# Performance work log

Hardware: AMD Instinct MI355X
Metric: run time of the kernel (lower is better)

Reference implementation:

```python
import jax, jax.numpy as jnp
import numpy as np

L = 2        # num_layers
D = 512      # d_model
H = 8        # heads
C = 512      # GAT per-head out channels (= d_model, concat=False -> mean over heads)
B, S, E = 4, 512, 4096
NEG = jnp.float32(-1e9)


def setup_inputs() -> dict:
    key = jax.random.key(0)
    ks = jax.random.split(key, 20)
    sc = 0.02  # weight init scale
    inp = {
        'x': jax.random.normal(ks[0], (B, S, D), jnp.float32),
        'Wq': jax.random.normal(ks[1], (L, D, D), jnp.float32) * sc,
        'bq': jnp.zeros((L, D), jnp.float32),
        'Wk': jax.random.normal(ks[2], (L, D, D), jnp.float32) * sc,
        'bk': jnp.zeros((L, D), jnp.float32),
        'Wv': jax.random.normal(ks[3], (L, D, D), jnp.float32) * sc,
        'bv': jnp.zeros((L, D), jnp.float32),
        'Wo': jax.random.normal(ks[4], (L, D, D), jnp.float32) * sc,
        'bo': jnp.zeros((L, D), jnp.float32),
        'gatW': jax.random.normal(ks[5], (L, D, H * C), jnp.float32) * sc,
        'att_src': jax.random.normal(ks[6], (L, H, C), jnp.float32) * sc,
        'att_dst': jax.random.normal(ks[7], (L, H, C), jnp.float32) * sc,
        'gat_bias': jnp.zeros((L, C), jnp.float32),
        'ln_g': jnp.ones((L, D), jnp.float32),
        'ln_b': jnp.zeros((L, D), jnp.float32),
        'input_len': jax.random.randint(ks[8], (B,), S // 2, S + 1, jnp.int32),
        'edges': jax.random.randint(ks[9], (B, 2, E), 0, S // 2, jnp.int32),
        'edge_num': jax.random.randint(ks[10], (B,), E // 2, E + 1, jnp.int32),
    }
    return inp


def layer_norm(x, g, b, eps=1e-5):
    m = x.mean(-1, keepdims=True)
    v = ((x - m) ** 2).mean(-1, keepdims=True)
    return (x - m) * jax.lax.rsqrt(v + eps) * g + b


def mha(x, pad_mask, Wq, bq, Wk, bk, Wv, bv, Wo, bo):
    # pad_mask: [B,S] True where padded (masked out)
    b, s, d = x.shape
    dh = d // H
    q = (x @ Wq + bq).reshape(b, s, H, dh)
    k = (x @ Wk + bk).reshape(b, s, H, dh)
    v = (x @ Wv + bv).reshape(b, s, H, dh)
    scores = jnp.einsum('bqhd,bkhd->bhqk', q, k) / jnp.float32(np.sqrt(dh))
    scores = jnp.where(pad_mask[:, None, None, :], NEG, scores)
    a = jax.nn.softmax(scores, axis=-1)
    o = jnp.einsum('bhqk,bkhd->bqhd', a, v).reshape(b, s, d)
    return o @ Wo + bo


def gat_single(x, edge_index, edge_mask, node_mask, W, a_src_w, a_dst_w, bias):
    # x: [S,D]; edge_index: [2,E]; GATConv(d_model,d_model,heads,concat=False)
    s = x.shape[0]
    h = (x @ W).reshape(s, H, C)
    a_src_n = (h * a_src_w).sum(-1)  # [S,H]
    a_dst_n = (h * a_dst_w).sum(-1)  # [S,H]
    # add self loops (PyG default) for valid nodes
    ar = jnp.arange(s, dtype=edge_index.dtype)
    src = jnp.concatenate([edge_index[0], ar])
    dst = jnp.concatenate([edge_index[1], ar])
    em = jnp.concatenate([edge_mask, node_mask])  # [E+S]
    alpha = jax.nn.leaky_relu(a_src_n[src] + a_dst_n[dst], 0.2)  # [E+S,H]
    alpha = jnp.where(em[:, None], alpha, NEG)
    amax = jax.ops.segment_max(alpha, dst, num_segments=s)  # [S,H]
    ex = jnp.exp(alpha - amax[dst]) * em[:, None].astype(alpha.dtype)
    denom = jax.ops.segment_sum(ex, dst, num_segments=s)
    coef = ex / (denom[dst] + 1e-16)
    msg = h[src] * coef[:, :, None]  # [E+S,H,C]
    out = jax.ops.segment_sum(msg, dst, num_segments=s)  # [S,H,C]
    return out.mean(axis=1) + bias  # concat=False -> mean over heads


def reference(x, Wq, bq, Wk, bk, Wv, bv, Wo, bo, gatW, att_src, att_dst,
              gat_bias, ln_g, ln_b, input_len, edges, edge_num):
    b, s, d = x.shape
    node_mask = jnp.arange(s)[None, :] < input_len[:, None]      # [B,S]
    edge_mask = jnp.arange(edges.shape[-1])[None, :] < edge_num[:, None]  # [B,E]
    pad_mask = ~node_mask
    out = x
    layer_outputs = []
    gat_b = jax.vmap(gat_single, in_axes=(0, 0, 0, 0, None, None, None, None))
    for i in range(L):
        out = mha(out, pad_mask, Wq[i], bq[i], Wk[i], bk[i], Wv[i], bv[i], Wo[i], bo[i])
        g = gat_b(out, edges, edge_mask, node_mask,
                  gatW[i], att_src[i], att_dst[i], gat_bias[i])
        y = jax.nn.relu(layer_norm(g, ln_g[i], ln_b[i])) + out
        out = jnp.where(node_mask[:, :, None], y, out)
        layer_outputs.append(out)
    return jnp.stack(layer_outputs)  # [L,B,S,D]
```

## Files before the change

kernel.cpp:

```cpp
#include <hip/hip_runtime.h>
#include <cstddef>

#define DMODEL 512
#define HEADS  8
#define DH     64
#define CCH    512
#define BATCH  4
#define SEQ    512
#define NEDGE  4096
#define NLAYER 2
#define HC     (HEADS*CCH)

typedef unsigned short bf16_t;
typedef __attribute__((ext_vector_type(8))) short short8;
typedef __attribute__((ext_vector_type(4))) float floatx4;

__device__ __forceinline__ bf16_t f2bf(float f){
  unsigned u = __float_as_uint(f);
  unsigned r = (u + 0x7FFFu + ((u>>16)&1u)) >> 16;
  return (bf16_t)r;
}
__device__ __forceinline__ float bf2f(bf16_t u){ return __uint_as_float(((unsigned)u)<<16); }

__global__ void k_f2b(const float* __restrict__ in, bf16_t* __restrict__ out, int n4){
  int i = blockIdx.x*256 + threadIdx.x;
  if (i < n4){
    float4 v = ((const float4*)in)[i];
    ushort4 o;
    o.x=f2bf(v.x); o.y=f2bf(v.y); o.z=f2bf(v.z); o.w=f2bf(v.w);
    ((ushort4*)out)[i]=o;
  }
}

__global__ __launch_bounds__(256) void k_edges(const int* __restrict__ edges,
    const int* __restrict__ edge_num, int* __restrict__ cnt, int* __restrict__ offs,
    int* __restrict__ elist, float* __restrict__ attn_nodes, int an_total){
  __shared__ int cnt_l[SEQ];
  __shared__ int off_l[SEQ];
  __shared__ int cur_l[SEQ];
  int b = blockIdx.x, tid = threadIdx.x;
  int chunk = an_total / BATCH;
  for (int i = tid; i < chunk; i += 256) attn_nodes[b*chunk + i] = 0.f;
  for (int s = tid; s < SEQ; s += 256) cnt_l[s] = 0;
  __syncthreads();
  int ne = edge_num[b];
  const int* dstrow = edges + (size_t)b*2*NEDGE + NEDGE;
  for (int e = tid; e < ne; e += 256) atomicAdd(&cnt_l[dstrow[e]], 1);
  __syncthreads();
  if (tid == 0){
    int acc = 0;
    for (int s = 0; s < SEQ; s++){ off_l[s] = acc; acc += cnt_l[s]; }
  }
  __syncthreads();
  for (int s = tid; s < SEQ; s += 256) cur_l[s] = off_l[s];
  __syncthreads();
  for (int e = tid; e < ne; e += 256){
    int dst = dstrow[e];
    int pos = atomicAdd(&cur_l[dst], 1);
    elist[(size_t)b*NEDGE + pos] = e;
  }
  for (int s = tid; s < SEQ; s += 256){
    cnt[b*SEQ + s]  = cnt_l[s];
    offs[b*SEQ + s] = off_l[s];
  }
}

struct WtJob { const float* W[10]; bf16_t* WT[10]; };
__global__ __launch_bounds__(256) void k_wt_all(WtJob j){
  __shared__ float T[32][65];
  int t = blockIdx.x, k0 = blockIdx.y*32;
  int wsel, n0, N;
  if (t < 64){ wsel = t>>3; n0 = (t&7)*64; N = 512; }
  else { int t2 = t-64; wsel = 8 + (t2>>6); n0 = (t2&63)*64; N = 4096; }
  const float* W = j.W[wsel];
  bf16_t* WT = j.WT[wsel];
  const int K = 512;
  int tid = threadIdx.x;
  int lk = tid>>3, ln = (tid&7)*8;
  const float* src = W + (size_t)(k0+lk)*N + n0 + ln;
  float4 v0 = *(const float4*)src;
  float4 v1 = *(const float4*)(src+4);
  T[lk][ln+0]=v0.x; T[lk][ln+1]=v0.y; T[lk][ln+2]=v0.z; T[lk][ln+3]=v0.w;
  T[lk][ln+4]=v1.x; T[lk][ln+5]=v1.y; T[lk][ln+6]=v1.z; T[lk][ln+7]=v1.w;
  __syncthreads();
  int wn = tid>>2, wk = (tid&3)*8;
  ushort4 o0, o1;
  o0.x=f2bf(T[wk+0][wn]); o0.y=f2bf(T[wk+1][wn]); o0.z=f2bf(T[wk+2][wn]); o0.w=f2bf(T[wk+3][wn]);
  o1.x=f2bf(T[wk+4][wn]); o1.y=f2bf(T[wk+5][wn]); o1.z=f2bf(T[wk+6][wn]); o1.w=f2bf(T[wk+7][wn]);
  bf16_t* dst = WT + (size_t)(n0+wn)*K + k0 + wk;
  *(ushort4*)dst = o0;
  *(ushort4*)(dst+4) = o1;
}

struct GemmB {
  const bf16_t* W; const float* bias; float* C; bf16_t* Cb;
  const float* att_s; const float* att_d; float* asrc; float* adst;
};
struct GemmB3 { GemmB g[3]; };

__global__ __launch_bounds__(256) void k_gemm_mfma(const bf16_t* __restrict__ A, GemmB3 p,
                                                   int N, int K){
  const GemmB& g = p.g[blockIdx.z];
  const bf16_t* Wt  = g.W;
  const float* bias = g.bias;
  float* C          = g.C;
  bf16_t* Cb        = g.Cb;
  __shared__ __align__(16) bf16_t As[2][64*64];
  __shared__ __align__(16) bf16_t Bs[2][64*64];
  int bm = blockIdx.x*64, bn = blockIdx.y*64;
  int tid = threadIdx.x;
  int wave = tid>>6, lane = tid&63;
  int wy = wave>>1, wx = wave&1;
  int quad = lane>>4, l16 = lane&15;
  int l7 = l16&7;
  floatx4 acc[2][2];
  #pragma unroll
  for (int i=0;i<2;i++)
    #pragma unroll
    for (int j=0;j<2;j++) acc[i][j] = (floatx4){0.f,0.f,0.f,0.f};
  int sr = tid>>2;
  int sch = (tid&3)*2;
  int sc = sch<<3;
  int wof0 = sr*64 + ((sch     ^ (sr&7))<<3);
  int wof1 = sr*64 + (((sch+1) ^ (sr&7))<<3);
  const bf16_t* Aptr = A  + (size_t)(bm+sr)*K + sc;
  const bf16_t* Bptr = Wt + (size_t)(bn+sr)*K + sc;
  uint4 a0, a1, b0, b1;
  a0 = *(const uint4*)(Aptr);     a1 = *(const uint4*)(Aptr + 8);
  b0 = *(const uint4*)(Bptr);     b1 = *(const uint4*)(Bptr + 8);
  *(uint4*)(As[0] + wof0) = a0;
  *(uint4*)(As[0] + wof1) = a1;
  *(uint4*)(Bs[0] + wof0) = b0;
  *(uint4*)(Bs[0] + wof1) = b1;
  int rch0 = (quad ^ l7)<<3;
  int rch1 = rch0 ^ 32;
  const int nk = K>>6;
  for (int k=0; k<nk; k++){
    __syncthreads();
    if (k+1 < nk){
      int ko = (k+1)<<6;
      a0 = *(const uint4*)(Aptr + ko);     a1 = *(const uint4*)(Aptr + ko + 8);
      b0 = *(const uint4*)(Bptr + ko);     b1 = *(const uint4*)(Bptr + ko + 8);
    }
    const bf16_t* Ab = As[k&1];
    const bf16_t* Bb = Bs[k&1];
    short8 af[2][2], bfr[2][2];
    #pragma unroll
    for (int i=0;i<2;i++){
      int ra = (wy*32+i*16+l16)*64;
      af[0][i] = *(const short8*)(Ab + ra + rch0);
      af[1][i] = *(const short8*)(Ab + ra + rch1);
    }
    #pragma unroll
    for (int j=0;j<2;j++){
      int rb = (wx*32+j*16+l16)*64;
      bfr[0][j] = *(const short8*)(Bb + rb + rch0);
      bfr[1][j] = *(const short8*)(Bb + rb + rch1);
    }
    #pragma unroll
    for (int i=0;i<2;i++)
      #pragma unroll
      for (int j=0;j<2;j++){
        acc[i][j] = __builtin_amdgcn_mfma_f32_16x16x32_bf16(af[0][i], bfr[0][j], acc[i][j], 0,0,0);
        acc[i][j] = __builtin_amdgcn_mfma_f32_16x16x32_bf16(af[1][i], bfr[1][j], acc[i][j], 0,0,0);
      }
    if (k+1 < nk){
      bf16_t* Aw = As[(k+1)&1];
      bf16_t* Bw = Bs[(k+1)&1];
      *(uint4*)(Aw + wof0) = a0;
      *(uint4*)(Aw + wof1) = a1;
      *(uint4*)(Bw + wof0) = b0;
      *(uint4*)(Bw + wof1) = b1;
    }
  }
  #pragma unroll
  for (int i=0;i<2;i++){
    int row = bm + wy*32 + i*16 + quad*4;
    #pragma unroll
    for (int j=0;j<2;j++){
      int col = bn + wx*32 + j*16 + l16;
      float bi = bias ? bias[col] : 0.f;
      #pragma unroll
      for (int r=0;r<4;r++){
        float vvv = acc[i][j][r] + bi;
        if (C)  C[(size_t)(row+r)*N + col] = vvv;
        if (Cb) Cb[(size_t)(row+r)*N + col] = f2bf(vvv);
      }
    }
  }
  if (g.asrc){
    int colbase = bn + wx*32;
    int hidx = colbase >> 9;
    float aw_s[2], aw_d[2];
    #pragma unroll
    for (int j=0;j<2;j++){
      int col = colbase + j*16 + l16;
      aw_s[j] = g.att_s[col];
      aw_d[j] = g.att_d[col];
    }
    #pragma unroll
    for (int i=0;i<2;i++){
      #pragma unroll
      for (int r=0;r<4;r++){
        float ps=0.f, pd=0.f;
        #pragma unroll
        for (int j=0;j<2;j++){ ps += acc[i][j][r]*aw_s[j]; pd += acc[i][j][r]*aw_d[j]; }
        #pragma unroll
        for (int m2=1;m2<16;m2<<=1){ ps += __shfl_xor(ps,m2); pd += __shfl_xor(pd,m2); }
        if (l16==0){
          int row = bm + wy*32 + i*16 + quad*4 + r;
          atomicAdd(&g.asrc[row*HEADS + hidx], ps);
          atomicAdd(&g.adst[row*HEADS + hidx], pd);
        }
      }
    }
  }
}

__global__ __launch_bounds__(256) void k_attn_flash(const bf16_t* __restrict__ q,
    const bf16_t* __restrict__ k, const bf16_t* __restrict__ v,
    const int* __restrict__ input_len, bf16_t* __restrict__ o){
  __shared__ __align__(16) bf16_t Kt[64*72];
  __shared__ __align__(16) bf16_t Vt[64*72];
  __shared__ __align__(16) bf16_t Pt[4][16*72];
  int q0 = blockIdx.x*64;
  int h  = blockIdx.y, b = blockIdx.z;
  int len = input_len[b];
  int tid = threadIdx.x;
  int w = tid>>6, lane = tid&63;
  int quad = lane>>4, l16 = lane&15;
  const bf16_t* qrow = q + ((size_t)(b*SEQ + q0 + w*16 + l16))*DMODEL + h*DH;
  short8 qa0 = *(const short8*)(qrow + quad*8);
  short8 qa1 = *(const short8*)(qrow + quad*8 + 32);
  int kr = tid>>2, kc = (tid&3)<<4;
  int vr = lane,   vc = w<<4;
  const bf16_t* kbase = k + ((size_t)(b*SEQ))*DMODEL + h*DH;
  const bf16_t* vbase = v + ((size_t)(b*SEQ))*DMODEL + h*DH;
  floatx4 oacc[4];
  #pragma unroll
  for (int dt=0;dt<4;dt++) oacc[dt] = (floatx4){0.f,0.f,0.f,0.f};
  float mrun[4], lrun[4];
  #pragma unroll
  for (int r=0;r<4;r++){ mrun[r]=-1e30f; lrun[r]=0.f; }
  for (int kt=0; kt<SEQ; kt+=64){
    if (kt >= len) break;
    uint4 kv0 = *(const uint4*)(kbase + (size_t)(kt+kr)*DMODEL + kc);
    uint4 kv1 = *(const uint4*)(kbase + (size_t)(kt+kr)*DMODEL + kc + 8);
    uint4 vv0 = *(const uint4*)(vbase + (size_t)(kt+vr)*DMODEL + vc);
    uint4 vv1 = *(const uint4*)(vbase + (size_t)(kt+vr)*DMODEL + vc + 8);
    __syncthreads();
    *(uint4*)(Kt + kr*72 + kc)     = kv0;
    *(uint4*)(Kt + kr*72 + kc + 8) = kv1;
    const ushort* vp0 = (const ushort*)&vv0;
    const ushort* vp1 = (const ushort*)&vv1;
    #pragma unroll
    for (int i2=0;i2<8;i2++) Vt[(vc+i2)*72 + vr]   = vp0[i2];
    #pragma unroll
    for (int i2=0;i2<8;i2++) Vt[(vc+8+i2)*72 + vr] = vp1[i2];
    __syncthreads();
    floatx4 sacc[4];
    #pragma unroll
    for (int nt=0;nt<4;nt++){
      sacc[nt] = (floatx4){0.f,0.f,0.f,0.f};
      short8 kb0 = *(const short8*)(Kt + (nt*16+l16)*72 + quad*8);
      short8 kb1 = *(const short8*)(Kt + (nt*16+l16)*72 + quad*8 + 32);
      sacc[nt] = __builtin_amdgcn_mfma_f32_16x16x32_bf16(qa0, kb0, sacc[nt], 0,0,0);
      sacc[nt] = __builtin_amdgcn_mfma_f32_16x16x32_bf16(qa1, kb1, sacc[nt], 0,0,0);
    }
    #pragma unroll
    for (int nt=0;nt<4;nt++){
      bool valid = (kt + nt*16 + l16) < len;
      #pragma unroll
      for (int r=0;r<4;r++){
        float sv = sacc[nt][r]*0.125f;
        sacc[nt][r] = valid ? sv : -1e30f;
      }
    }
    float alpha[4];
    #pragma unroll
    for (int r=0;r<4;r++){
      float mx = fmaxf(fmaxf(sacc[0][r],sacc[1][r]), fmaxf(sacc[2][r],sacc[3][r]));
      #pragma unroll
      for (int off=1; off<16; off<<=1) mx = fmaxf(mx, __shfl_xor(mx, off));
      float mn = fmaxf(mrun[r], mx);
      alpha[r] = __expf(mrun[r]-mn);
      mrun[r] = mn;
      float rs = 0.f;
      #pragma unroll
      for (int nt=0;nt<4;nt++){
        float pp = __expf(sacc[nt][r]-mn);
        sacc[nt][r] = pp; rs += pp;
      }
      #pragma unroll
      for (int off=1; off<16; off<<=1) rs += __shfl_xor(rs, off);
      lrun[r] = lrun[r]*alpha[r] + rs;
    }
    #pragma unroll
    for (int dt=0;dt<4;dt++)
      #pragma unroll
      for (int r=0;r<4;r++) oacc[dt][r] *= alpha[r];
    bf16_t* pw = Pt[w];
    #pragma unroll
    for (int nt=0;nt<4;nt++)
      #pragma unroll
      for (int r=0;r<4;r++) pw[(quad*4+r)*72 + nt*16 + l16] = f2bf(sacc[nt][r]);
    short8 pa0 = *(const short8*)(pw + l16*72 + quad*8);
    short8 pa1 = *(const short8*)(pw + l16*72 + quad*8 + 32);
    #pragma unroll
    for (int dt=0;dt<4;dt++){
      short8 vb0 = *(const short8*)(Vt + (dt*16+l16)*72 + quad*8);
      short8 vb1 = *(const short8*)(Vt + (dt*16+l16)*72 + quad*8 + 32);
      oacc[dt] = __builtin_amdgcn_mfma_f32_16x16x32_bf16(pa0, vb0, oacc[dt], 0,0,0);
      oacc[dt] = __builtin_amdgcn_mfma_f32_16x16x32_bf16(pa1, vb1, oacc[dt], 0,0,0);
    }
  }
  bf16_t* obase = o + ((size_t)(b*SEQ + q0 + w*16 + quad*4))*DMODEL + h*DH;
  #pragma unroll
  for (int r=0;r<4;r++){
    float invl = 1.f/lrun[r];
    #pragma unroll
    for (int dt=0;dt<4;dt++)
      obase[(size_t)r*DMODEL + dt*16 + l16] = f2bf(oacc[dt][r]*invl);
  }
}

__global__ __launch_bounds__(256) void k_gat_ln(const bf16_t* __restrict__ hbuf,
    const float* __restrict__ asrc, const float* __restrict__ adst,
    const int* __restrict__ offs, const int* __restrict__ cnt, const int* __restrict__ elist,
    const int* __restrict__ edges, const int* __restrict__ input_len,
    const float* __restrict__ gat_bias, const float* __restrict__ mha,
    const float* __restrict__ lng, const float* __restrict__ lnb,
    bf16_t* __restrict__ curb, float* __restrict__ outp){
  int s = blockIdx.x, b = blockIdx.y;
  int tid = threadIdx.x;
  size_t row = ((size_t)(b*SEQ+s))*DMODEL;
  int c0 = tid*2;
  float2 xv = *(const float2*)(mha + row + c0);
  if (s >= input_len[b]){
    curb[row+c0]   = f2bf(xv.x);
    curb[row+c0+1] = f2bf(xv.y);
    *(float2*)(outp + row + c0) = xv;
    return;
  }
  __shared__ float amax_s[8], den_s[8], adl[8];
  __shared__ float cf[32][8];
  __shared__ int   cs[32];
  __shared__ float red[256];
  int n = cnt[b*SEQ+s];
  const int* el = elist + (size_t)b*NEDGE + offs[b*SEQ+s];
  const int* srcrow = edges + (size_t)b*2*NEDGE;
  if (tid < 8) adl[tid] = adst[(b*SEQ+s)*HEADS + tid];
  __syncthreads();
  if (tid < 64){
    float mx[8];
    #pragma unroll
    for (int h2=0;h2<8;h2++) mx[h2] = -1e30f;
    for (int j = tid; j <= n; j += 64){
      int src = (j==n) ? s : srcrow[el[j]];
      const float* ap = asrc + (size_t)(b*SEQ+src)*HEADS;
      #pragma unroll
      for (int h2=0;h2<8;h2++){
        float a = ap[h2] + adl[h2];
        a = (a>0.f)? a : 0.2f*a;
        mx[h2] = fmaxf(mx[h2], a);
      }
    }
    #pragma unroll
    for (int h2=0;h2<8;h2++){
      float vmx = mx[h2];
      #pragma unroll
      for (int off=32; off; off>>=1) vmx = fmaxf(vmx, __shfl_xor(vmx,off,64));
      mx[h2]=vmx;
    }
    float sm[8];
    #pragma unroll
    for (int h2=0;h2<8;h2++) sm[h2]=0.f;
    for (int j = tid; j <= n; j += 64){
      int src = (j==n) ? s : srcrow[el[j]];
      const float* ap = asrc + (size_t)(b*SEQ+src)*HEADS;
      #pragma unroll
      for (int h2=0;h2<8;h2++){
        float a = ap[h2] + adl[h2];
        a = (a>0.f)? a : 0.2f*a;
        sm[h2] += __expf(a - mx[h2]);
      }
    }
    #pragma unroll
    for (int h2=0;h2<8;h2++){
      float vs = sm[h2];
      #pragma unroll
      for (int off=32; off; off>>=1) vs += __shfl_xor(vs,off,64);
      if (tid==0){ amax_s[h2]=mx[h2]; den_s[h2]=vs; }
    }
  }
  __syncthreads();
  float acc0=0.f, acc1=0.f;
  for (int j0=0; j0 <= n; j0 += 32){
    int jm = min(32, n+1-j0);
    if (tid < jm*8){
      int jj = j0 + (tid>>3), h2 = tid&7;
      int src = (jj==n) ? s : srcrow[el[jj]];
      if (h2==0) cs[tid>>3] = src;
      float a = asrc[(size_t)(b*SEQ+src)*HEADS + h2] + adl[h2];
      a = (a>0.f)? a : 0.2f*a;
      cf[tid>>3][h2] = __expf(a - amax_s[h2]) / (den_s[h2] + 1e-16f);
    }
    __syncthreads();
    for (int jj=0; jj<jm; ++jj){
      int src = cs[jj];
      const bf16_t* hrow = hbuf + ((size_t)(b*SEQ+src))*HC;
      #pragma unroll
      for (int h2=0;h2<8;h2++){
        float wgt = cf[jj][h2];
        ushort2 hv = *(const ushort2*)(hrow + h2*CCH + c0);
        acc0 += wgt * bf2f(hv.x);
        acc1 += wgt * bf2f(hv.y);
      }
    }
    __syncthreads();
  }
  float g0 = acc0*0.125f + gat_bias[c0];
  float g1 = acc1*0.125f + gat_bias[c0+1];
  red[tid] = g0+g1;
  __syncthreads();
  for (int off=128; off; off>>=1){ if (tid<off) red[tid]+=red[tid+off]; __syncthreads(); }
  float mean = red[0]*(1.f/512.f);
  __syncthreads();
  float d0 = g0-mean, d1 = g1-mean;
  red[tid] = d0*d0 + d1*d1;
  __syncthreads();
  for (int off=128; off; off>>=1){ if (tid<off) red[tid]+=red[tid+off]; __syncthreads(); }
  float inv = rsqrtf(red[0]*(1.f/512.f) + 1e-5f);
  float t0 = d0*inv*lng[c0]   + lnb[c0];
  float t1 = d1*inv*lng[c0+1] + lnb[c0+1];
  float y0 = fmaxf(t0,0.f) + xv.x;
  float y1 = fmaxf(t1,0.f) + xv.y;
  curb[row+c0]   = f2bf(y0);
  curb[row+c0+1] = f2bf(y1);
  float2 outv = { y0, y1 };
  *(float2*)(outp + row + c0) = outv;
}

extern "C" void kernel_launch(void* const* d_in, const int* in_sizes, int n_in,
                              void* d_out, int out_size, void* d_ws, size_t ws_size,
                              hipStream_t stream){
  (void)in_sizes; (void)n_in; (void)out_size; (void)ws_size;
  const float* x       = (const float*)d_in[0];
  const float* Wq      = (const float*)d_in[1];
  const float* bq      = (const float*)d_in[2];
  const float* Wk      = (const float*)d_in[3];
  const float* bk      = (const float*)d_in[4];
  const float* Wv      = (const float*)d_in[5];
  const float* bv      = (const float*)d_in[6];
  const float* Wo      = (const float*)d_in[7];
  const float* bo      = (const float*)d_in[8];
  const float* gatW    = (const float*)d_in[9];
  const float* att_src = (const float*)d_in[10];
  const float* att_dst = (const float*)d_in[11];
  const float* gat_bias= (const float*)d_in[12];
  const float* ln_g    = (const float*)d_in[13];
  const float* ln_b    = (const float*)d_in[14];
  const int* input_len  = (const int*)d_in[15];
  const int* edges      = (const int*)d_in[16];
  const int* edge_num   = (const int*)d_in[17];
  float* outp = (float*)d_out;

  char* w = (char*)d_ws;
  size_t off = 0;
  auto alloc = [&](size_t bytes)->char*{ char* p = w + off; off += (bytes + 255) & ~(size_t)255; return p; };
  const size_t BSD = (size_t)BATCH*SEQ*DMODEL;
  const size_t BSH = (size_t)BATCH*SEQ*HEADS;
  float* mha  = (float*)alloc(BSD*4);
  bf16_t* hb  = (bf16_t*)alloc((size_t)BATCH*SEQ*HC*2);
  float* attn_nodes = (float*)alloc((size_t)NLAYER*2*BSH*4);
  int* cnt    = (int*)alloc(BATCH*SEQ*4);
  int* offs   = (int*)alloc(BATCH*SEQ*4);
  int* elist  = (int*)alloc((size_t)BATCH*NEDGE*4);
  bf16_t* xbf  = (bf16_t*)alloc(BSD*2);
  bf16_t* curb = (bf16_t*)alloc(BSD*2);
  bf16_t* qbf  = (bf16_t*)alloc(BSD*2);
  bf16_t* kbf  = (bf16_t*)alloc(BSD*2);
  bf16_t* vbf  = (bf16_t*)alloc(BSD*2);
  bf16_t* obf  = (bf16_t*)alloc(BSD*2);
  bf16_t* abf  = (bf16_t*)alloc(BSD*2);
  bf16_t* wqt  = (bf16_t*)alloc((size_t)NLAYER*DMODEL*DMODEL*2);
  bf16_t* wkt  = (bf16_t*)alloc((size_t)NLAYER*DMODEL*DMODEL*2);
  bf16_t* wvt  = (bf16_t*)alloc((size_t)NLAYER*DMODEL*DMODEL*2);
  bf16_t* wot  = (bf16_t*)alloc((size_t)NLAYER*DMODEL*DMODEL*2);
  bf16_t* gwt  = (bf16_t*)alloc((size_t)NLAYER*DMODEL*HC*2);

  k_edges<<<dim3(BATCH),256,0,stream>>>(edges, edge_num, cnt, offs, elist,
                                        attn_nodes, (int)(NLAYER*2*BSH));
  WtJob wj;
  for (int i=0;i<NLAYER;i++){
    size_t wo = (size_t)i*DMODEL*DMODEL;
    wj.W[i*4+0]=Wq+wo;  wj.WT[i*4+0]=wqt+wo;
    wj.W[i*4+1]=Wk+wo;  wj.WT[i*4+1]=wkt+wo;
    wj.W[i*4+2]=Wv+wo;  wj.WT[i*4+2]=wvt+wo;
    wj.W[i*4+3]=Wo+wo;  wj.WT[i*4+3]=wot+wo;
    size_t go = (size_t)i*DMODEL*HC;
    wj.W[8+i]=gatW+go;  wj.WT[8+i]=gwt+go;
  }
  k_wt_all<<<dim3(192, 16),256,0,stream>>>(wj);
  k_f2b<<<dim3((unsigned)(BSD/4/256)),256,0,stream>>>(x, xbf, (int)(BSD/4));

  const int M = BATCH*SEQ;
  for (int i=0;i<NLAYER;i++){
    size_t wo = (size_t)i*DMODEL*DMODEL;
    size_t bo2 = (size_t)i*DMODEL;
    float* asrc = attn_nodes + (size_t)i*2*BSH;
    float* adst = asrc + BSH;
    const bf16_t* Ab = (i==0) ? xbf : curb;
    GemmB3 qkv;
    qkv.g[0] = { wqt+wo, bq+bo2, nullptr, qbf, nullptr, nullptr, nullptr, nullptr };
    qkv.g[1] = { wkt+wo, bk+bo2, nullptr, kbf, nullptr, nullptr, nullptr, nullptr };
    qkv.g[2] = { wvt+wo, bv+bo2, nullptr, vbf, nullptr, nullptr, nullptr, nullptr };
    k_gemm_mfma<<<dim3(M/64, DMODEL/64, 3),256,0,stream>>>(Ab, qkv, DMODEL, DMODEL);
    k_attn_flash<<<dim3(SEQ/64, HEADS, BATCH),256,0,stream>>>(qbf, kbf, vbf, input_len, obf);
    GemmB3 og;
    og.g[0] = { wot+wo, bo+bo2, mha, abf, nullptr, nullptr, nullptr, nullptr };
    og.g[1] = og.g[0]; og.g[2] = og.g[0];
    k_gemm_mfma<<<dim3(M/64, DMODEL/64, 1),256,0,stream>>>(obf, og, DMODEL, DMODEL);
    GemmB3 gg;
    gg.g[0] = { gwt + (size_t)i*DMODEL*HC, nullptr, nullptr, hb,
                att_src + (size_t)i*HC, att_dst + (size_t)i*HC, asrc, adst };
    gg.g[1] = gg.g[0]; gg.g[2] = gg.g[0];
    k_gemm_mfma<<<dim3(M/64, HC/64, 1),256,0,stream>>>(abf, gg, HC, DMODEL);
    k_gat_ln<<<dim3(SEQ, BATCH),256,0,stream>>>(hb, asrc, adst, offs, cnt, elist, edges,
        input_len, gat_bias + (size_t)i*CCH, mha, ln_g+bo2, ln_b+bo2,
        curb, outp + (size_t)i*BSD);
  }
}
```

Baseline: 313.8 us.

## Split attention keys across warp pairs and merge preprocessing kernels into one launch

```diff
diff --git a/kernel.cpp b/kernel.cpp
--- a/kernel.cpp
+++ b/kernel.cpp
@@ -22,74 +22,75 @@
 }
 __device__ __forceinline__ float bf2f(bf16_t u){ return __uint_as_float(((unsigned)u)<<16); }
 
-__global__ void k_f2b(const float* __restrict__ in, bf16_t* __restrict__ out, int n4){
-  int i = blockIdx.x*256 + threadIdx.x;
-  if (i < n4){
-    float4 v = ((const float4*)in)[i];
-    ushort4 o;
-    o.x=f2bf(v.x); o.y=f2bf(v.y); o.z=f2bf(v.z); o.w=f2bf(v.w);
-    ((ushort4*)out)[i]=o;
-  }
-}
-
-__global__ __launch_bounds__(256) void k_edges(const int* __restrict__ edges,
+struct WtJob { const float* W[10]; bf16_t* WT[10]; };
+__global__ __launch_bounds__(256) void k_pre(const int* __restrict__ edges,
     const int* __restrict__ edge_num, int* __restrict__ cnt, int* __restrict__ offs,
-    int* __restrict__ elist, float* __restrict__ attn_nodes, int an_total){
+    int* __restrict__ elist, float* __restrict__ attn_nodes, int an_total,
+    WtJob j, const float* __restrict__ x, bf16_t* __restrict__ xbf, int n4){
   __shared__ int cnt_l[SEQ];
   __shared__ int off_l[SEQ];
   __shared__ int cur_l[SEQ];
-  int b = blockIdx.x, tid = threadIdx.x;
-  int chunk = an_total / BATCH;
-  for (int i = tid; i < chunk; i += 256) attn_nodes[b*chunk + i] = 0.f;
-  for (int s = tid; s < SEQ; s += 256) cnt_l[s] = 0;
-  __syncthreads();
-  int ne = edge_num[b];
-  const int* dstrow = edges + (size_t)b*2*NEDGE + NEDGE;
-  for (int e = tid; e < ne; e += 256) atomicAdd(&cnt_l[dstrow[e]], 1);
-  __syncthreads();
-  if (tid == 0){
-    int acc = 0;
-    for (int s = 0; s < SEQ; s++){ off_l[s] = acc; acc += cnt_l[s]; }
-  }
-  __syncthreads();
-  for (int s = tid; s < SEQ; s += 256) cur_l[s] = off_l[s];
-  __syncthreads();
-  for (int e = tid; e < ne; e += 256){
-    int dst = dstrow[e];
-    int pos = atomicAdd(&cur_l[dst], 1);
-    elist[(size_t)b*NEDGE + pos] = e;
-  }
-  for (int s = tid; s < SEQ; s += 256){
-    cnt[b*SEQ + s]  = cnt_l[s];
-    offs[b*SEQ + s] = off_l[s];
-  }
-}
-
-struct WtJob { const float* W[10]; bf16_t* WT[10]; };
-__global__ __launch_bounds__(256) void k_wt_all(WtJob j){
   __shared__ float T[32][65];
-  int t = blockIdx.x, k0 = blockIdx.y*32;
-  int wsel, n0, N;
-  if (t < 64){ wsel = t>>3; n0 = (t&7)*64; N = 512; }
-  else { int t2 = t-64; wsel = 8 + (t2>>6); n0 = (t2&63)*64; N = 4096; }
-  const float* W = j.W[wsel];
-  bf16_t* WT = j.WT[wsel];
-  const int K = 512;
-  int tid = threadIdx.x;
-  int lk = tid>>3, ln = (tid&7)*8;
-  const float* src = W + (size_t)(k0+lk)*N + n0 + ln;
-  float4 v0 = *(const float4*)src;
-  float4 v1 = *(const float4*)(src+4);
-  T[lk][ln+0]=v0.x; T[lk][ln+1]=v0.y; T[lk][ln+2]=v0.z; T[lk][ln+3]=v0.w;
-  T[lk][ln+4]=v1.x; T[lk][ln+5]=v1.y; T[lk][ln+6]=v1.z; T[lk][ln+7]=v1.w;
-  __syncthreads();
-  int wn = tid>>2, wk = (tid&3)*8;
-  ushort4 o0, o1;
-  o0.x=f2bf(T[wk+0][wn]); o0.y=f2bf(T[wk+1][wn]); o0.z=f2bf(T[wk+2][wn]); o0.w=f2bf(T[wk+3][wn]);
-  o1.x=f2bf(T[wk+4][wn]); o1.y=f2bf(T[wk+5][wn]); o1.z=f2bf(T[wk+6][wn]); o1.w=f2bf(T[wk+7][wn]);
-  bf16_t* dst = WT + (size_t)(n0+wn)*K + k0 + wk;
-  *(ushort4*)dst = o0;
-  *(ushort4*)(dst+4) = o1;
+  int bz = blockIdx.x, tid = threadIdx.x;
+  if (bz < 4){
+    int b = bz;
+    int chunk = an_total / BATCH;
+    for (int i = tid; i < chunk; i += 256) attn_nodes[b*chunk + i] = 0.f;
+    for (int s = tid; s < SEQ; s += 256) cnt_l[s] = 0;
+    __syncthreads();
+    int ne = edge_num[b];
+    const int* dstrow = edges + (size_t)b*2*NEDGE + NEDGE;
+    for (int e = tid; e < ne; e += 256) atomicAdd(&cnt_l[dstrow[e]], 1);
+    __syncthreads();
+    if (tid == 0){
+      int acc = 0;
+      for (int s = 0; s < SEQ; s++){ off_l[s] = acc; acc += cnt_l[s]; }
+    }
+    __syncthreads();
+    for (int s = tid; s < SEQ; s += 256) cur_l[s] = off_l[s];
+    __syncthreads();
+    for (int e = tid; e < ne; e += 256){
+      int dst = dstrow[e];
+      int pos = atomicAdd(&cur_l[dst], 1);
+      elist[(size_t)b*NEDGE + pos] = e;
+    }
+    for (int s = tid; s < SEQ; s += 256){
+      cnt[b*SEQ + s]  = cnt_l[s];
+      offs[b*SEQ + s] = off_l[s];
+    }
+  } else if (bz < 4+3072){
+    int idx = bz - 4;
+    int t = idx >> 4;
+    int k0 = (idx & 15)*32;
+    int wsel, n0, N;
+    if (t < 64){ wsel = t>>3; n0 = (t&7)*64; N = 512; }
+    else { int t2 = t-64; wsel = 8 + (t2>>6); n0 = (t2&63)*64; N = 4096; }
+    const float* W = j.W[wsel];
+    bf16_t* WT = j.WT[wsel];
+    const int K = 512;
+    int lk = tid>>3, ln = (tid&7)*8;
+    const float* src = W + (size_t)(k0+lk)*N + n0 + ln;
+    float4 v0 = *(const float4*)src;
+    float4 v1 = *(const float4*)(src+4);
+    T[lk][ln+0]=v0.x; T[lk][ln+1]=v0.y; T[lk][ln+2]=v0.z; T[lk][ln+3]=v0.w;
+    T[lk][ln+4]=v1.x; T[lk][ln+5]=v1.y; T[lk][ln+6]=v1.z; T[lk][ln+7]=v1.w;
+    __syncthreads();
+    int wn = tid>>2, wk = (tid&3)*8;
+    ushort4 o0, o1;
+    o0.x=f2bf(T[wk+0][wn]); o0.y=f2bf(T[wk+1][wn]); o0.z=f2bf(T[wk+2][wn]); o0.w=f2bf(T[wk+3][wn]);
+    o1.x=f2bf(T[wk+4][wn]); o1.y=f2bf(T[wk+5][wn]); o1.z=f2bf(T[wk+6][wn]); o1.w=f2bf(T[wk+7][wn]);
+    bf16_t* dst = WT + (size_t)(n0+wn)*K + k0 + wk;
+    *(ushort4*)dst = o0;
+    *(ushort4*)(dst+4) = o1;
+  } else {
+    int i = (bz-3076)*256 + tid;
+    if (i < n4){
+      float4 v = ((const float4*)x)[i];
+      ushort4 o;
+      o.x=f2bf(v.x); o.y=f2bf(v.y); o.z=f2bf(v.z); o.w=f2bf(v.w);
+      ((ushort4*)xbf)[i]=o;
+    }
+  }
 }
 
 struct GemmB {
@@ -220,20 +221,25 @@
 __global__ __launch_bounds__(256) void k_attn_flash(const bf16_t* __restrict__ q,
     const bf16_t* __restrict__ k, const bf16_t* __restrict__ v,
     const int* __restrict__ input_len, bf16_t* __restrict__ o){
-  __shared__ __align__(16) bf16_t Kt[64*72];
-  __shared__ __align__(16) bf16_t Vt[64*72];
+  __shared__ __align__(16) bf16_t Kt[2][64*72];
+  __shared__ __align__(16) bf16_t Vt[2][64*72];
   __shared__ __align__(16) bf16_t Pt[4][16*72];
-  int q0 = blockIdx.x*64;
+  __shared__ float Om[2][16*64];
+  __shared__ float Ml[2][2][16];
+  int q0 = blockIdx.x*32;
   int h  = blockIdx.y, b = blockIdx.z;
   int len = input_len[b];
   int tid = threadIdx.x;
   int w = tid>>6, lane = tid&63;
   int quad = lane>>4, l16 = lane&15;
-  const bf16_t* qrow = q + ((size_t)(b*SEQ + q0 + w*16 + l16))*DMODEL + h*DH;
+  int rg = w>>1, kh = w&1;
+  const bf16_t* qrow = q + ((size_t)(b*SEQ + q0 + rg*16 + l16))*DMODEL + h*DH;
   short8 qa0 = *(const short8*)(qrow + quad*8);
   short8 qa1 = *(const short8*)(qrow + quad*8 + 32);
-  int kr = tid>>2, kc = (tid&3)<<4;
-  int vr = lane,   vc = w<<4;
+  int sg = tid>>7;
+  int st = tid & 127;
+  int kr = st>>1,  kc = (st&1)*32;
+  int vrr = st&63, vcc = (st>>6)*32;
   const bf16_t* kbase = k + ((size_t)(b*SEQ))*DMODEL + h*DH;
   const bf16_t* vbase = v + ((size_t)(b*SEQ))*DMODEL + h*DH;
   floatx4 oacc[4];
@@ -242,34 +248,36 @@
   float mrun[4], lrun[4];
   #pragma unroll
   for (int r=0;r<4;r++){ mrun[r]=-1e30f; lrun[r]=0.f; }
-  for (int kt=0; kt<SEQ; kt+=64){
-    if (kt >= len) break;
-    uint4 kv0 = *(const uint4*)(kbase + (size_t)(kt+kr)*DMODEL + kc);
-    uint4 kv1 = *(const uint4*)(kbase + (size_t)(kt+kr)*DMODEL + kc + 8);
-    uint4 vv0 = *(const uint4*)(vbase + (size_t)(kt+vr)*DMODEL + vc);
-    uint4 vv1 = *(const uint4*)(vbase + (size_t)(kt+vr)*DMODEL + vc + 8);
-    __syncthreads();
-    *(uint4*)(Kt + kr*72 + kc)     = kv0;
-    *(uint4*)(Kt + kr*72 + kc + 8) = kv1;
-    const ushort* vp0 = (const ushort*)&vv0;
-    const ushort* vp1 = (const ushort*)&vv1;
-    #pragma unroll
-    for (int i2=0;i2<8;i2++) Vt[(vc+i2)*72 + vr]   = vp0[i2];
-    #pragma unroll
-    for (int i2=0;i2<8;i2++) Vt[(vc+8+i2)*72 + vr] = vp1[i2];
-    __syncthreads();
+  for (int t=0; t<4; t++){
+    int ktg = sg*256 + t*64;
+    uint4 kv[4], vv[4];
+    #pragma unroll
+    for (int c=0;c<4;c++) kv[c] = *(const uint4*)(kbase + (size_t)(ktg+kr)*DMODEL + kc + c*8);
+    #pragma unroll
+    for (int c=0;c<4;c++) vv[c] = *(const uint4*)(vbase + (size_t)(ktg+vrr)*DMODEL + vcc + c*8);
+    __syncthreads();
+    #pragma unroll
+    for (int c=0;c<4;c++) *(uint4*)(Kt[sg] + kr*72 + kc + c*8) = kv[c];
+    #pragma unroll
+    for (int c=0;c<4;c++){
+      const ushort* vp = (const ushort*)&vv[c];
+      #pragma unroll
+      for (int i2=0;i2<8;i2++) Vt[sg][(vcc + c*8 + i2)*72 + vrr] = vp[i2];
+    }
+    __syncthreads();
+    int kabs_base = kh*256 + t*64;
     floatx4 sacc[4];
     #pragma unroll
     for (int nt=0;nt<4;nt++){
       sacc[nt] = (floatx4){0.f,0.f,0.f,0.f};
-      short8 kb0 = *(const short8*)(Kt + (nt*16+l16)*72 + quad*8);
-      short8 kb1 = *(const short8*)(Kt + (nt*16+l16)*72 + quad*8 + 32);
+      short8 kb0 = *(const short8*)(Kt[kh] + (nt*16+l16)*72 + quad*8);
+      short8 kb1 = *(const short8*)(Kt[kh] + (nt*16+l16)*72 + quad*8 + 32);
       sacc[nt] = __builtin_amdgcn_mfma_f32_16x16x32_bf16(qa0, kb0, sacc[nt], 0,0,0);
       sacc[nt] = __builtin_amdgcn_mfma_f32_16x16x32_bf16(qa1, kb1, sacc[nt], 0,0,0);
     }
     #pragma unroll
     for (int nt=0;nt<4;nt++){
-      bool valid = (kt + nt*16 + l16) < len;
+      bool valid = (kabs_base + nt*16 + l16) < len;
       #pragma unroll
       for (int r=0;r<4;r++){
         float sv = sacc[nt][r]*0.125f;
@@ -308,19 +316,43 @@
     short8 pa1 = *(const short8*)(pw + l16*72 + quad*8 + 32);
     #pragma unroll
     for (int dt=0;dt<4;dt++){
-      short8 vb0 = *(const short8*)(Vt + (dt*16+l16)*72 + quad*8);
-      short8 vb1 = *(const short8*)(Vt + (dt*16+l16)*72 + quad*8 + 32);
+      short8 vb0 = *(const short8*)(Vt[kh] + (dt*16+l16)*72 + quad*8);
+      short8 vb1 = *(const short8*)(Vt[kh] + (dt*16+l16)*72 + quad*8 + 32);
       oacc[dt] = __builtin_amdgcn_mfma_f32_16x16x32_bf16(pa0, vb0, oacc[dt], 0,0,0);
       oacc[dt] = __builtin_amdgcn_mfma_f32_16x16x32_bf16(pa1, vb1, oacc[dt], 0,0,0);
     }
   }
-  bf16_t* obase = o + ((size_t)(b*SEQ + q0 + w*16 + quad*4))*DMODEL + h*DH;
-  #pragma unroll
-  for (int r=0;r<4;r++){
-    float invl = 1.f/lrun[r];
+  __syncthreads();
+  if (kh==1){
     #pragma unroll
     for (int dt=0;dt<4;dt++)
-      obase[(size_t)r*DMODEL + dt*16 + l16] = f2bf(oacc[dt][r]*invl);
+      #pragma unroll
+      for (int r=0;r<4;r++) Om[rg][(quad*4+r)*64 + dt*16 + l16] = oacc[dt][r];
+    if (l16==0){
+      #pragma unroll
+      for (int r=0;r<4;r++){ Ml[rg][0][quad*4+r]=mrun[r]; Ml[rg][1][quad*4+r]=lrun[r]; }
+    }
+  }
+  __syncthreads();
+  if (kh==0){
+    float a0[4], a1[4], invl[4];
+    #pragma unroll
+    for (int r=0;r<4;r++){
+      float m1 = Ml[rg][0][quad*4+r];
+      float l1 = Ml[rg][1][quad*4+r];
+      float m  = fmaxf(mrun[r], m1);
+      a0[r] = __expf(mrun[r]-m);
+      a1[r] = __expf(m1-m);
+      invl[r] = 1.f/(lrun[r]*a0[r] + l1*a1[r]);
+    }
+    bf16_t* obase = o + ((size_t)(b*SEQ + q0 + rg*16 + quad*4))*DMODEL + h*DH;
+    #pragma unroll
+    for (int r=0;r<4;r++)
+      #pragma unroll
+      for (int dt=0;dt<4;dt++){
+        float val = (oacc[dt][r]*a0[r] + Om[rg][(quad*4+r)*64 + dt*16 + l16]*a1[r])*invl[r];
+        obase[(size_t)r*DMODEL + dt*16 + l16] = f2bf(val);
+      }
   }
 }
 
@@ -489,8 +521,6 @@
   bf16_t* wot  = (bf16_t*)alloc((size_t)NLAYER*DMODEL*DMODEL*2);
   bf16_t* gwt  = (bf16_t*)alloc((size_t)NLAYER*DMODEL*HC*2);
 
-  k_edges<<<dim3(BATCH),256,0,stream>>>(edges, edge_num, cnt, offs, elist,
-                                        attn_nodes, (int)(NLAYER*2*BSH));
   WtJob wj;
   for (int i=0;i<NLAYER;i++){
     size_t wo = (size_t)i*DMODEL*DMODEL;
@@ -501,8 +531,8 @@
     size_t go = (size_t)i*DMODEL*HC;
     wj.W[8+i]=gatW+go;  wj.WT[8+i]=gwt+go;
   }
-  k_wt_all<<<dim3(192, 16),256,0,stream>>>(wj);
-  k_f2b<<<dim3((unsigned)(BSD/4/256)),256,0,stream>>>(x, xbf, (int)(BSD/4));
+  k_pre<<<dim3(4+3072+1024),256,0,stream>>>(edges, edge_num, cnt, offs, elist,
+      attn_nodes, (int)(NLAYER*2*BSH), wj, x, xbf, (int)(BSD/4));
 
   const int M = BATCH*SEQ;
   for (int i=0;i<NLAYER;i++){
@@ -516,7 +546,7 @@
     qkv.g[1] = { wkt+wo, bk+bo2, nullptr, kbf, nullptr, nullptr, nullptr, nullptr };
     qkv.g[2] = { wvt+wo, bv+bo2, nullptr, vbf, nullptr, nullptr, nullptr, nullptr };
     k_gemm_mfma<<<dim3(M/64, DMODEL/64, 3),256,0,stream>>>(Ab, qkv, DMODEL, DMODEL);
-    k_attn_flash<<<dim3(SEQ/64, HEADS, BATCH),256,0,stream>>>(qbf, kbf, vbf, input_len, obf);
+    k_attn_flash<<<dim3(SEQ/32, HEADS, BATCH),256,0,stream>>>(qbf, kbf, vbf, input_len, obf);
     GemmB3 og;
     og.g[0] = { wot+wo, bo+bo2, mha, abf, nullptr, nullptr, nullptr, nullptr };
     og.g[1] = og.g[0]; og.g[2] = og.g[0];
```

Measured after the change: 318.6 us. Within noise of the previous version (+1.5%).
